# Performance work log

Measured on AMD Instinct MI355X. Metric: run time of the kernel, lower is better.

## Reference

```python
import jax, jax.numpy as jnp
import numpy as np

LENGTHS = [1024, 768, 896, 512, 1024, 640, 1024, 768, 512, 896, 1024, 704]  # sum = 9792
EMBED, HEADS = 1024, 16
HDIM = EMBED // HEADS  # 64
ROPE_BASE = 10000.0


def _rotate_half(x):
    half = x.shape[-1] // 2
    return jnp.concatenate([-x[..., half:], x[..., :half]], axis=-1)


def setup_inputs() -> dict:
    key = jax.random.key(0)
    ks = jax.random.split(key, 8)
    T = sum(LENGTHS)
    hidden = jax.random.normal(ks[0], (T, EMBED), jnp.float32)
    # RoPE cos/sin: positions restart at 0 within each packed segment
    pos = np.concatenate([np.arange(l) for l in LENGTHS]).astype(np.float32)  # [T]
    inv_freq = 1.0 / (ROPE_BASE ** (np.arange(0, HDIM, 2, dtype=np.float32) / HDIM))
    freqs = np.outer(pos, inv_freq)                       # [T, HDIM//2]
    emb = np.concatenate([freqs, freqs], axis=-1)         # [T, HDIM]
    cos = jnp.asarray(np.cos(emb), jnp.float32)
    sin = jnp.asarray(np.sin(emb), jnp.float32)
    s = 0.02
    q_w = jax.random.normal(ks[1], (EMBED, EMBED), jnp.float32) * s
    k_w = jax.random.normal(ks[2], (EMBED, EMBED), jnp.float32) * s
    v_w = jax.random.normal(ks[3], (EMBED, EMBED), jnp.float32) * s
    out_w = jax.random.normal(ks[4], (EMBED, EMBED), jnp.float32) * s
    q_b = jax.random.normal(ks[5], (EMBED,), jnp.float32) * s
    v_b = jax.random.normal(ks[6], (EMBED,), jnp.float32) * s
    out_b = jax.random.normal(ks[7], (EMBED,), jnp.float32) * s
    return {
        "hidden_states": hidden, "cos": cos, "sin": sin,
        "q_w": q_w, "q_b": q_b, "k_w": k_w, "v_w": v_w, "v_b": v_b,
        "out_w": out_w, "out_b": out_b,
        "seq_len": jnp.array(LENGTHS, jnp.int32),
        "max_seqlen": 1024,
    }


def reference(hidden_states, cos, sin, q_w, q_b, k_w, v_w, v_b, out_w, out_b,
              seq_len, max_seqlen):
    T, D = hidden_states.shape
    H, Dh = HEADS, D // HEADS
    B = seq_len.shape[0]
    L = max_seqlen  # static python int

    # Projections (torch Linear: y = x @ W.T + b; k_proj has no bias)
    q = (hidden_states @ q_w.T + q_b).reshape(T, H, Dh)
    k = (hidden_states @ k_w.T).reshape(T, H, Dh)
    v = (hidden_states @ v_w.T + v_b).reshape(T, H, Dh)

    # Inline RoPE (cos/sin broadcast over heads)
    c = cos[:, None, :]
    s = sin[:, None, :]
    q = q * c + _rotate_half(q) * s
    k = k * c + _rotate_half(k) * s

    # Gather packed tokens into padded [B, L, H, Dh] (honors ragged structure:
    # no [T, T] dense score matrix, only per-segment [L, L] blocks)
    cu = jnp.concatenate([jnp.zeros((1,), seq_len.dtype), jnp.cumsum(seq_len)])[:-1]  # [B] starts
    ar = jnp.arange(L)
    idx = cu[:, None] + ar[None, :]                 # [B, L] token ids
    valid = ar[None, :] < seq_len[:, None]          # [B, L]
    idxc = jnp.minimum(idx, T - 1)
    qp = q[idxc]                                    # [B, L, H, Dh]
    kp = k[idxc]
    vp = v[idxc]

    scale = 1.0 / jnp.sqrt(jnp.float32(Dh))
    scores = jnp.einsum('blhd,bmhd->bhlm', qp, kp) * scale  # [B, H, L, L]
    causal = ar[:, None] >= ar[None, :]             # [L, L]
    mask = valid[:, None, None, :] & causal[None, None, :, :]
    scores = jnp.where(mask, scores, jnp.float32(-1e30))
    probs = jax.nn.softmax(scores, axis=-1)
    attn = jnp.einsum('bhlm,bmhd->blhd', probs, vp).reshape(B, L, D)

    # Scatter valid tokens back to packed layout [T, D]
    attn = attn * valid[..., None].astype(attn.dtype)
    flat = jnp.zeros((T, D), attn.dtype).at[idxc.reshape(-1)].add(attn.reshape(-1, D))
    return flat @ out_w.T + out_b
```

## Files before the change

kernel.cpp:

```cpp
#include <hip/hip_runtime.h>

typedef __bf16 bf16;
typedef __bf16 bf16x8 __attribute__((ext_vector_type(8)));
typedef __bf16 bf16x4 __attribute__((ext_vector_type(4)));
typedef float  f32x4  __attribute__((ext_vector_type(4)));

#define T_TOTAL 9792
#define EMBED   1024
#define NHEAD   16
#define HDIM    64

__constant__ int c_seq_start[12] = {0,1024,1792,2688,3200,4224,4864,5888,6656,7168,8064,9088};
__constant__ int c_tiles_cum[13] = {0,16,28,42,50,66,76,92,104,112,126,142,153};

typedef __attribute__((address_space(1))) unsigned int gu32;
typedef __attribute__((address_space(3))) unsigned int lu32;

__device__ __forceinline__ void load_lds16(const void* g, void* l) {
    __builtin_amdgcn_global_load_lds((gu32*)g, (lu32*)l, 16, 0, 0);
}

__device__ __forceinline__ f32x4 mfma16(bf16x8 a, bf16x8 b, f32x4 c) {
    return __builtin_amdgcn_mfma_f32_16x16x32_bf16(a, b, c, 0, 0, 0);
}

struct CvtArgs {
    const void* src[10];
    bf16*       dst[10];
    int         n[10];
    int         cum[10];
};

__global__ void to_bf16_fused(CvtArgs a, const unsigned short* __restrict__ disc)
{
    const bool f32 = (disc[0] == 0);
    const int blk = blockIdx.x;
    int seg = 0;
    #pragma unroll
    for (int i = 1; i < 10; ++i) if (blk >= a.cum[i]) seg = i;
    int i0 = (blk - a.cum[seg]) * 2048 + threadIdx.x * 8;
    if (i0 >= a.n[seg]) return;
    bf16x8 o;
    if (f32) {
        const float4* s = (const float4*)((const float*)a.src[seg] + i0);
        float4 x = s[0], y = s[1];
        o[0]=(bf16)x.x; o[1]=(bf16)x.y; o[2]=(bf16)x.z; o[3]=(bf16)x.w;
        o[4]=(bf16)y.x; o[5]=(bf16)y.y; o[6]=(bf16)y.z; o[7]=(bf16)y.w;
    } else {
        o = *(const bf16x8*)((const bf16*)a.src[seg] + i0);
    }
    *(bf16x8*)(a.dst[seg] + i0) = o;
}

__device__ __forceinline__
void gemm_core(const bf16* __restrict__ A, const bf16* __restrict__ W,
               int M, int m0, int n0, f32x4 (&acc)[4][4],
               bf16* lA, bf16* lB)
{
    const int tid  = threadIdx.x;
    const int wave = tid >> 6, lane = tid & 63;
    const int lrow = lane >> 3;
    const int gsw  = (lane & 7) ^ lrow;
    const int ln   = lane & 15, lq = lane >> 4;
    const int e7   = ln & 7;
    const int wm = (wave & 1) * 64,  wn = (wave >> 1) * 64;

    for (int k0 = 0; k0 < 1024; k0 += 64) {
        __syncthreads();
        for (int j = 0; j < 4; ++j) {
            int r = j * 32 + wave * 8;
            int gr = m0 + r + lrow; if (gr > M - 1) gr = M - 1;
            load_lds16(A + (size_t)gr * EMBED + k0 + gsw * 8, &lA[r * 64]);
            load_lds16(W + (size_t)(n0 + r + lrow) * EMBED + k0 + gsw * 8, &lB[r * 64]);
        }
        __syncthreads();
        #pragma unroll
        for (int kb = 0; kb < 2; ++kb) {
            bf16x8 af[4], bfr[4];
            #pragma unroll
            for (int i = 0; i < 4; ++i)
                af[i]  = *(const bf16x8*)&lA[(wm + i * 16 + ln) * 64 + (((kb * 4 + lq) ^ e7) * 8)];
            #pragma unroll
            for (int i = 0; i < 4; ++i)
                bfr[i] = *(const bf16x8*)&lB[(wn + i * 16 + ln) * 64 + (((kb * 4 + lq) ^ e7) * 8)];
            #pragma unroll
            for (int mi = 0; mi < 4; ++mi)
                #pragma unroll
                for (int ni = 0; ni < 4; ++ni)
                    acc[mi][ni] = mfma16(af[mi], bfr[ni], acc[mi][ni]);
        }
    }
}

__device__ __forceinline__ void map_block(int L, int NY, int& x, int& y)
{
    const int per = 8 * NY;
    const int full = 9 * per;
    if (L < full) { int sc = L / per, rem = L % per; x = sc * 8 + (rem & 7); y = rem >> 3; }
    else          { int rem = L - full; x = 72 + rem % 5; y = rem / 5; }
}

__global__ __launch_bounds__(256, 2)
void gemm_qkv(const bf16* __restrict__ A,
              const bf16* __restrict__ Wq, const bf16* __restrict__ Wk,
              const bf16* __restrict__ Wv, const bf16* __restrict__ qb,
              const bf16* __restrict__ vb,
              const bf16* __restrict__ cosb, const bf16* __restrict__ sinb,
              bf16* __restrict__ Cq, bf16* __restrict__ Ck,
              bf16* __restrict__ Vt, int M)
{
    __shared__ __align__(16) bf16 lA[128 * 64];
    __shared__ __align__(16) bf16 lB[128 * 64];

    int x, yy;
    map_block(blockIdx.x, 24, x, yy);
    const int which = yy >> 3;
    const int m0 = x * 128, n0 = (yy & 7) * 128;

    const bf16* W = (which == 0) ? Wq : (which == 1) ? Wk : Wv;
    f32x4 acc[4][4] = {};
    gemm_core(A, W, M, m0, n0, acc, lA, lB);

    const int tid  = threadIdx.x;
    const int wave = tid >> 6, lane = tid & 63;
    const int ln   = lane & 15, lq = lane >> 4;
    const int wm = (wave & 1) * 64,  wn = (wave >> 1) * 64;

    if (which < 2) {
        bf16* C = (which == 0) ? Cq : Ck;
        const bf16* bias = (which == 0) ? qb : nullptr;
        #pragma unroll
        for (int mi = 0; mi < 4; ++mi) {
            int trow = m0 + wm + mi * 16 + lq * 4;
            if (trow >= M) continue;
            #pragma unroll
            for (int ni = 0; ni < 2; ++ni) {
                int d    = ni * 16 + ln;
                int col0 = n0 + wn + d;
                int col1 = col0 + 32;
                float b0 = bias ? (float)bias[col0] : 0.0f;
                float b1 = bias ? (float)bias[col1] : 0.0f;
                #pragma unroll
                for (int r = 0; r < 4; ++r) {
                    int t = trow + r;
                    float c = (float)cosb[t * HDIM + d];
                    float s = (float)sinb[t * HDIM + d];
                    float x0 = acc[mi][ni][r] + b0;
                    float x1 = acc[mi][ni + 2][r] + b1;
                    C[(size_t)t * EMBED + col0] = (bf16)(x0 * c - x1 * s);
                    C[(size_t)t * EMBED + col1] = (bf16)(x1 * c + x0 * s);
                }
            }
        }
    } else {
        const int hd0 = n0 + wn;
        #pragma unroll
        for (int mi = 0; mi < 4; ++mi) {
            int trow = m0 + wm + mi * 16 + lq * 4;
            if (trow >= M) continue;
            #pragma unroll
            for (int ni = 0; ni < 4; ++ni) {
                int d = ni * 16 + ln;
                float bv = (float)vb[hd0 + d];
                bf16x4 o;
                #pragma unroll
                for (int r = 0; r < 4; ++r) o[r] = (bf16)(acc[mi][ni][r] + bv);
                *(bf16x4*)&Vt[(size_t)(hd0 + d) * T_TOTAL + trow] = o;
            }
        }
    }
}

__global__ __launch_bounds__(256, 2)
void gemm_out(const bf16* __restrict__ A, const bf16* __restrict__ W,
              const bf16* __restrict__ bias, void* __restrict__ out, int M,
              const unsigned short* __restrict__ disc)
{
    __shared__ __align__(16) bf16 lA[128 * 64];
    __shared__ __align__(16) bf16 lB[128 * 64];

    int x, yy;
    map_block(blockIdx.x, 8, x, yy);
    const int m0 = x * 128, n0 = yy * 128;

    f32x4 acc[4][4] = {};
    gemm_core(A, W, M, m0, n0, acc, lA, lB);

    const bool f32 = (disc[0] == 0);
    const int tid  = threadIdx.x;
    const int wave = tid >> 6, lane = tid & 63;
    const int ln   = lane & 15, lq = lane >> 4;
    const int wm = (wave & 1) * 64,  wn = (wave >> 1) * 64;

    #pragma unroll
    for (int mi = 0; mi < 4; ++mi) {
        int trow = m0 + wm + mi * 16 + lq * 4;
        if (trow >= M) continue;
        #pragma unroll
        for (int ni = 0; ni < 4; ++ni) {
            int col = n0 + wn + ni * 16 + ln;
            float bv = (float)bias[col];
            #pragma unroll
            for (int r = 0; r < 4; ++r) {
                float v = acc[mi][ni][r] + bv;
                size_t idx = (size_t)(trow + r) * EMBED + col;
                if (f32) ((float*)out)[idx] = v;
                else     ((bf16*)out)[idx]  = (bf16)v;
            }
        }
    }
}

__global__ __launch_bounds__(256, 3)
void attn_kernel(const bf16* __restrict__ Q, const bf16* __restrict__ K,
                 const bf16* __restrict__ Vt, bf16* __restrict__ O)
{
    __shared__ __align__(16) bf16 sK[2][64 * 64];
    __shared__ __align__(16) bf16 sV[2][64 * 64];
    __shared__ __align__(16) bf16 sQP[4 * 16 * 72];

    const int tid  = threadIdx.x;
    const int wave = tid >> 6, lane = tid & 63;
    const int lrow = lane >> 3;
    const int gsw  = (lane & 7) ^ lrow;
    const int ln   = lane & 15, lq = lane >> 4;
    const int e7   = ln & 7;
    const int h = blockIdx.y;

    int b = 0;
    #pragma unroll
    for (int i = 1; i < 13; ++i) if ((int)blockIdx.x >= c_tiles_cum[i]) b = i;
    const int qt = blockIdx.x - c_tiles_cum[b];
    const int t0 = c_seq_start[b] + qt * 64;
    const int kvb0 = c_seq_start[b];

    for (int p = 0; p < 2; ++p) {
        int r = p * 32 + wave * 8;
        load_lds16(Q  + (size_t)(t0 + r + lrow) * EMBED + h * HDIM + gsw * 8, &sQP[r * 64]);
        load_lds16(K  + (size_t)(kvb0 + r + lrow) * EMBED + h * HDIM + gsw * 8, &sK[0][r * 64]);
        load_lds16(Vt + (size_t)(h * HDIM + r + lrow) * T_TOTAL + kvb0 + gsw * 8, &sV[0][r * 64]);
    }

    bf16x8 qf[2];
    f32x4 oacc[4] = {};
    float m_i = -1e30f, l_i = 0.0f;
    const float sc = 0.125f * 1.44269504088896f;
    const int q_loc = wave * 16 + ln;
    bf16* sP = &sQP[wave * 16 * 72];

    for (int j = 0; j <= qt; ++j) {
        __syncthreads();
        const int cur = j & 1;
        if (j == 0) {
            qf[0] = *(const bf16x8*)&sQP[q_loc * 64 + ((0 + lq) ^ e7) * 8];
            qf[1] = *(const bf16x8*)&sQP[q_loc * 64 + ((4 + lq) ^ e7) * 8];
            __syncthreads();
        }
        if (j < qt) {
            const int kvb = kvb0 + (j + 1) * 64;
            const int nxt = cur ^ 1;
            for (int p = 0; p < 2; ++p) {
                int r = p * 32 + wave * 8;
                load_lds16(K  + (size_t)(kvb + r + lrow) * EMBED + h * HDIM + gsw * 8, &sK[nxt][r * 64]);
                load_lds16(Vt + (size_t)(h * HDIM + r + lrow) * T_TOTAL + kvb + gsw * 8, &sV[nxt][r * 64]);
            }
        }

        f32x4 s[4] = {};
        #pragma unroll
        for (int kk = 0; kk < 2; ++kk)
            #pragma unroll
            for (int ni = 0; ni < 4; ++ni) {
                bf16x8 kf = *(const bf16x8*)&sK[cur][(ni * 16 + ln) * 64 + (((kk * 4 + lq) ^ e7) * 8)];
                s[ni] = mfma16(kf, qf[kk], s[ni]);
            }

        float pb[4][4];
        if (j == qt) {
            #pragma unroll
            for (int ni = 0; ni < 4; ++ni)
                #pragma unroll
                for (int r = 0; r < 4; ++r) {
                    int kv = ni * 16 + lq * 4 + r;
                    pb[ni][r] = (kv <= q_loc) ? s[ni][r] * sc : -1e30f;
                }
        } else {
            #pragma unroll
            for (int ni = 0; ni < 4; ++ni)
                #pragma unroll
                for (int r = 0; r < 4; ++r)
                    pb[ni][r] = s[ni][r] * sc;
        }

        float mx = pb[0][0];
        #pragma unroll
        for (int ni = 0; ni < 4; ++ni)
            #pragma unroll
            for (int r = 0; r < 4; ++r) mx = fmaxf(mx, pb[ni][r]);
        mx = fmaxf(mx, __shfl_xor(mx, 16));
        mx = fmaxf(mx, __shfl_xor(mx, 32));
        float mnew  = fmaxf(m_i, mx);
        float alpha = exp2f(m_i - mnew);
        m_i = mnew;

        float rs = 0.0f;
        #pragma unroll
        for (int ni = 0; ni < 4; ++ni)
            #pragma unroll
            for (int r = 0; r < 4; ++r) {
                float pe = exp2f(pb[ni][r] - mnew);
                pb[ni][r] = pe;
                rs += pe;
            }
        rs += __shfl_xor(rs, 16);
        rs += __shfl_xor(rs, 32);
        l_i = l_i * alpha + rs;
        #pragma unroll
        for (int d = 0; d < 4; ++d)
            #pragma unroll
            for (int r = 0; r < 4; ++r) oacc[d][r] *= alpha;

        #pragma unroll
        for (int ni = 0; ni < 4; ++ni) {
            bf16x4 w4;
            #pragma unroll
            for (int r = 0; r < 4; ++r) w4[r] = (bf16)pb[ni][r];
            *(bf16x4*)&sP[ln * 72 + ni * 16 + lq * 4] = w4;
        }
        asm volatile("s_waitcnt lgkmcnt(0)" ::: "memory");

        #pragma unroll
        for (int kk = 0; kk < 2; ++kk) {
            bf16x8 pf = *(const bf16x8*)&sP[ln * 72 + kk * 32 + lq * 8];
            #pragma unroll
            for (int d = 0; d < 4; ++d) {
                bf16x8 vf = *(const bf16x8*)&sV[cur][(d * 16 + ln) * 64 + (((kk * 4 + lq) ^ e7) * 8)];
                oacc[d] = mfma16(vf, pf, oacc[d]);
            }
        }
    }

    const float inv = 1.0f / l_i;
    const size_t row = (size_t)(t0 + q_loc) * EMBED + h * HDIM;
    #pragma unroll
    for (int d = 0; d < 4; ++d) {
        bf16x4 o4;
        #pragma unroll
        for (int r = 0; r < 4; ++r) o4[r] = (bf16)(oacc[d][r] * inv);
        *(bf16x4*)&O[row + d * 16 + lq * 4] = o4;
    }
}

extern "C" void kernel_launch(void* const* d_in, const int* in_sizes, int n_in,
                              void* d_out, int out_size, void* d_ws, size_t ws_size,
                              hipStream_t stream)
{
    const unsigned short* disc = (const unsigned short*)d_in[1];

    const size_t SZ  = (size_t)T_TOTAL * EMBED;
    const size_t CS  = (size_t)T_TOTAL * HDIM;
    const size_t WSZ = (size_t)EMBED * EMBED;

    bf16* p = (bf16*)d_ws;
    bf16* ch   = p; p += SZ;
    bf16* ccos = p; p += CS;
    bf16* csin = p; p += CS;
    bf16* cqw  = p; p += WSZ;
    bf16* ckw  = p; p += WSZ;
    bf16* cvw  = p; p += WSZ;
    bf16* cow  = p; p += WSZ;
    bf16* cqb  = p; p += EMBED;
    bf16* cvb  = p; p += EMBED;
    bf16* cob  = p; p += EMBED;
    bf16* wq   = p; p += SZ;
    bf16* wk   = p; p += SZ;
    bf16* wvt  = p; p += SZ;

    CvtArgs ca;
    const void* srcs[10] = {d_in[0], d_in[1], d_in[2], d_in[3], d_in[5],
                            d_in[6], d_in[8], d_in[4], d_in[7], d_in[9]};
    bf16* dsts[10] = {ch, ccos, csin, cqw, ckw, cvw, cow, cqb, cvb, cob};
    int   ns[10]   = {(int)SZ, (int)CS, (int)CS, (int)WSZ, (int)WSZ,
                      (int)WSZ, (int)WSZ, EMBED, EMBED, EMBED};
    int cum = 0;
    for (int i = 0; i < 10; ++i) {
        ca.src[i] = srcs[i]; ca.dst[i] = dsts[i]; ca.n[i] = ns[i];
        ca.cum[i] = cum;
        cum += (ns[i] + 2047) / 2048;
    }
    to_bf16_fused<<<cum, 256, 0, stream>>>(ca, disc);

    gemm_qkv<<<77 * 24, 256, 0, stream>>>(ch, cqw, ckw, cvw, cqb, cvb,
                                          ccos, csin, wq, wk, wvt, T_TOTAL);
    attn_kernel<<<dim3(153, 16), 256, 0, stream>>>(wq, wk, wvt, wq);
    gemm_out<<<77 * 8, 256, 0, stream>>>(wq, cow, cob, d_out, T_TOTAL, disc);
}
```

Measured before the change: 297.0 us.

## Use 256x256 double-buffered GEMM tiles with 8 waves for QKV and output projections

Both projection GEMMs move from 128x128 tiles on 4 waves to 256x256 tiles on 8 waves. LDS is double-buffered so the next K-slice is prefetched during the MFMA phases, and MFMA issue is raised with setprio. The aim is more operand reuse per byte loaded and less barrier/load latency exposed. In exchange the grids shrink sharply (156 blocks for the output GEMM), 128 KB of LDS limits each CU to one block, and tail waves may leave CUs idle.

```diff
diff --git a/kernel.cpp b/kernel.cpp
--- a/kernel.cpp
+++ b/kernel.cpp
@@ -52,10 +52,23 @@
     *(bf16x8*)(a.dst[seg] + i0) = o;
 }
 
+__device__ __forceinline__ void map_block2(int L, int NX, int NY, int& x, int& y)
+{
+    const int per = 8 * NY;
+    const int nfull = NX >> 3;
+    const int full = nfull * per;
+    if (L < full) { int sc = L / per, rem = L % per; x = sc * 8 + (rem & 7); y = rem >> 3; }
+    else {
+        int rem = L - full;
+        int tw = NX - nfull * 8;
+        x = nfull * 8 + rem % tw; y = rem / tw;
+    }
+}
+
 __device__ __forceinline__
-void gemm_core(const bf16* __restrict__ A, const bf16* __restrict__ W,
-               int M, int m0, int n0, f32x4 (&acc)[4][4],
-               bf16* lA, bf16* lB)
+void gemm_core256(const bf16* __restrict__ A, const bf16* __restrict__ W,
+                  int M, int m0, int n0, f32x4 (&acc)[8][4],
+                  bf16* lA, bf16* lB)
 {
     const int tid  = threadIdx.x;
     const int wave = tid >> 6, lane = tid & 63;
@@ -63,44 +76,66 @@
     const int gsw  = (lane & 7) ^ lrow;
     const int ln   = lane & 15, lq = lane >> 4;
     const int e7   = ln & 7;
-    const int wm = (wave & 1) * 64,  wn = (wave >> 1) * 64;
-
-    for (int k0 = 0; k0 < 1024; k0 += 64) {
-        __syncthreads();
+    const int wm   = (wave >> 2) & 1;
+    const int wn   = wave & 3;
+
+    auto stage = [&](int kt, int buf) {
+        const int k0 = kt * 64;
+        bf16* dA = lA + buf * (256 * 64);
+        bf16* dB = lB + buf * (256 * 64);
+        #pragma unroll
         for (int j = 0; j < 4; ++j) {
-            int r = j * 32 + wave * 8;
+            int r = j * 64 + wave * 8;
             int gr = m0 + r + lrow; if (gr > M - 1) gr = M - 1;
-            load_lds16(A + (size_t)gr * EMBED + k0 + gsw * 8, &lA[r * 64]);
-            load_lds16(W + (size_t)(n0 + r + lrow) * EMBED + k0 + gsw * 8, &lB[r * 64]);
-        }
-        __syncthreads();
-        #pragma unroll
-        for (int kb = 0; kb < 2; ++kb) {
-            bf16x8 af[4], bfr[4];
-            #pragma unroll
-            for (int i = 0; i < 4; ++i)
-                af[i]  = *(const bf16x8*)&lA[(wm + i * 16 + ln) * 64 + (((kb * 4 + lq) ^ e7) * 8)];
-            #pragma unroll
-            for (int i = 0; i < 4; ++i)
-                bfr[i] = *(const bf16x8*)&lB[(wn + i * 16 + ln) * 64 + (((kb * 4 + lq) ^ e7) * 8)];
-            #pragma unroll
-            for (int mi = 0; mi < 4; ++mi)
-                #pragma unroll
-                for (int ni = 0; ni < 4; ++ni)
-                    acc[mi][ni] = mfma16(af[mi], bfr[ni], acc[mi][ni]);
-        }
-    }
-}
-
-__device__ __forceinline__ void map_block(int L, int NY, int& x, int& y)
-{
-    const int per = 8 * NY;
-    const int full = 9 * per;
-    if (L < full) { int sc = L / per, rem = L % per; x = sc * 8 + (rem & 7); y = rem >> 3; }
-    else          { int rem = L - full; x = 72 + rem % 5; y = rem / 5; }
-}
-
-__global__ __launch_bounds__(256, 2)
+            load_lds16(A + (size_t)gr * EMBED + k0 + gsw * 8, dA + r * 64);
+            load_lds16(W + (size_t)(n0 + r + lrow) * EMBED + k0 + gsw * 8, dB + r * 64);
+        }
+    };
+
+    stage(0, 0);
+    __syncthreads();
+
+    for (int kt = 0; kt < 16; ++kt) {
+        const int p = kt & 1;
+        const bf16* sA = lA + p * (256 * 64);
+        const bf16* sB = lB + p * (256 * 64);
+        #pragma unroll
+        for (int ph = 0; ph < 4; ++ph) {
+            const int mh = ph >> 1, nh = ph & 1;
+            if (ph == 0 && kt + 1 < 16) stage(kt + 1, p ^ 1);
+
+            bf16x8 af[2][4], bfr[2][2];
+            #pragma unroll
+            for (int kb = 0; kb < 2; ++kb) {
+                #pragma unroll
+                for (int mi = 0; mi < 4; ++mi)
+                    af[kb][mi] = *(const bf16x8*)
+                        &sA[(wm * 128 + mh * 64 + mi * 16 + ln) * 64 + (((kb * 4 + lq) ^ e7) * 8)];
+                #pragma unroll
+                for (int niq = 0; niq < 2; ++niq)
+                    bfr[kb][niq] = *(const bf16x8*)
+                        &sB[(wn * 64 + nh * 32 + niq * 16 + ln) * 64 + (((kb * 4 + lq) ^ e7) * 8)];
+            }
+            __builtin_amdgcn_s_barrier();
+            asm volatile("s_waitcnt lgkmcnt(0)" ::: "memory");
+            __builtin_amdgcn_s_setprio(1);
+            #pragma unroll
+            for (int kb = 0; kb < 2; ++kb)
+                #pragma unroll
+                for (int mi = 0; mi < 4; ++mi)
+                    #pragma unroll
+                    for (int niq = 0; niq < 2; ++niq)
+                        acc[mh * 4 + mi][nh * 2 + niq] =
+                            mfma16(af[kb][mi], bfr[kb][niq], acc[mh * 4 + mi][nh * 2 + niq]);
+            __builtin_amdgcn_s_setprio(0);
+            if (ph == 3 && kt + 1 < 16)
+                asm volatile("s_waitcnt vmcnt(0)" ::: "memory");
+            __builtin_amdgcn_s_barrier();
+        }
+    }
+}
+
+__global__ __launch_bounds__(512, 2)
 void gemm_qkv(const bf16* __restrict__ A,
               const bf16* __restrict__ Wq, const bf16* __restrict__ Wk,
               const bf16* __restrict__ Wv, const bf16* __restrict__ qb,
@@ -109,34 +144,36 @@
               bf16* __restrict__ Cq, bf16* __restrict__ Ck,
               bf16* __restrict__ Vt, int M)
 {
-    __shared__ __align__(16) bf16 lA[128 * 64];
-    __shared__ __align__(16) bf16 lB[128 * 64];
+    __shared__ __align__(16) bf16 lA[2 * 256 * 64];
+    __shared__ __align__(16) bf16 lB[2 * 256 * 64];
 
     int x, yy;
-    map_block(blockIdx.x, 24, x, yy);
-    const int which = yy >> 3;
-    const int m0 = x * 128, n0 = (yy & 7) * 128;
+    map_block2(blockIdx.x, 39, 12, x, yy);
+    const int which = yy >> 2;
+    const int m0 = x * 256, n0 = (yy & 3) * 256;
 
     const bf16* W = (which == 0) ? Wq : (which == 1) ? Wk : Wv;
-    f32x4 acc[4][4] = {};
-    gemm_core(A, W, M, m0, n0, acc, lA, lB);
+    f32x4 acc[8][4] = {};
+    gemm_core256(A, W, M, m0, n0, acc, lA, lB);
 
     const int tid  = threadIdx.x;
     const int wave = tid >> 6, lane = tid & 63;
     const int ln   = lane & 15, lq = lane >> 4;
-    const int wm = (wave & 1) * 64,  wn = (wave >> 1) * 64;
+    const int wm   = (wave >> 2) & 1, wn = wave & 3;
+    const int rbase = m0 + wm * 128;
+    const int cbase = n0 + wn * 64;
 
     if (which < 2) {
         bf16* C = (which == 0) ? Cq : Ck;
         const bf16* bias = (which == 0) ? qb : nullptr;
         #pragma unroll
-        for (int mi = 0; mi < 4; ++mi) {
-            int trow = m0 + wm + mi * 16 + lq * 4;
+        for (int mi = 0; mi < 8; ++mi) {
+            int trow = rbase + mi * 16 + lq * 4;
             if (trow >= M) continue;
             #pragma unroll
             for (int ni = 0; ni < 2; ++ni) {
                 int d    = ni * 16 + ln;
-                int col0 = n0 + wn + d;
+                int col0 = cbase + d;
                 int col1 = col0 + 32;
                 float b0 = bias ? (float)bias[col0] : 0.0f;
                 float b1 = bias ? (float)bias[col1] : 0.0f;
@@ -153,52 +190,53 @@
             }
         }
     } else {
-        const int hd0 = n0 + wn;
-        #pragma unroll
-        for (int mi = 0; mi < 4; ++mi) {
-            int trow = m0 + wm + mi * 16 + lq * 4;
+        #pragma unroll
+        for (int mi = 0; mi < 8; ++mi) {
+            int trow = rbase + mi * 16 + lq * 4;
             if (trow >= M) continue;
             #pragma unroll
             for (int ni = 0; ni < 4; ++ni) {
                 int d = ni * 16 + ln;
-                float bv = (float)vb[hd0 + d];
+                float bv = (float)vb[cbase + d];
                 bf16x4 o;
                 #pragma unroll
                 for (int r = 0; r < 4; ++r) o[r] = (bf16)(acc[mi][ni][r] + bv);
-                *(bf16x4*)&Vt[(size_t)(hd0 + d) * T_TOTAL + trow] = o;
-            }
-        }
-    }
-}
-
-__global__ __launch_bounds__(256, 2)
+                *(bf16x4*)&Vt[(size_t)(cbase + d) * T_TOTAL + trow] = o;
+            }
+        }
+    }
+}
+
+__global__ __launch_bounds__(512, 2)
 void gemm_out(const bf16* __restrict__ A, const bf16* __restrict__ W,
               const bf16* __restrict__ bias, void* __restrict__ out, int M,
               const unsigned short* __restrict__ disc)
 {
-    __shared__ __align__(16) bf16 lA[128 * 64];
-    __shared__ __align__(16) bf16 lB[128 * 64];
+    __shared__ __align__(16) bf16 lA[2 * 256 * 64];
+    __shared__ __align__(16) bf16 lB[2 * 256 * 64];
 
     int x, yy;
-    map_block(blockIdx.x, 8, x, yy);
-    const int m0 = x * 128, n0 = yy * 128;
-
-    f32x4 acc[4][4] = {};
-    gemm_core(A, W, M, m0, n0, acc, lA, lB);
+    map_block2(blockIdx.x, 39, 4, x, yy);
+    const int m0 = x * 256, n0 = yy * 256;
+
+    f32x4 acc[8][4] = {};
+    gemm_core256(A, W, M, m0, n0, acc, lA, lB);
 
     const bool f32 = (disc[0] == 0);
     const int tid  = threadIdx.x;
     const int wave = tid >> 6, lane = tid & 63;
     const int ln   = lane & 15, lq = lane >> 4;
-    const int wm = (wave & 1) * 64,  wn = (wave >> 1) * 64;
+    const int wm   = (wave >> 2) & 1, wn = wave & 3;
+    const int rbase = m0 + wm * 128;
+    const int cbase = n0 + wn * 64;
 
     #pragma unroll
-    for (int mi = 0; mi < 4; ++mi) {
-        int trow = m0 + wm + mi * 16 + lq * 4;
+    for (int mi = 0; mi < 8; ++mi) {
+        int trow = rbase + mi * 16 + lq * 4;
         if (trow >= M) continue;
         #pragma unroll
         for (int ni = 0; ni < 4; ++ni) {
-            int col = n0 + wn + ni * 16 + ln;
+            int col = cbase + ni * 16 + ln;
             float bv = (float)bias[col];
             #pragma unroll
             for (int r = 0; r < 4; ++r) {
@@ -390,8 +428,8 @@
     }
     to_bf16_fused<<<cum, 256, 0, stream>>>(ca, disc);
 
-    gemm_qkv<<<77 * 24, 256, 0, stream>>>(ch, cqw, ckw, cvw, cqb, cvb,
+    gemm_qkv<<<39 * 12, 512, 0, stream>>>(ch, cqw, ckw, cvw, cqb, cvb,
                                           ccos, csin, wq, wk, wvt, T_TOTAL);
     attn_kernel<<<dim3(153, 16), 256, 0, stream>>>(wq, wk, wvt, wq);
-    gemm_out<<<77 * 8, 256, 0, stream>>>(wq, cow, cob, d_out, T_TOTAL, disc);
-}
+    gemm_out<<<39 * 4, 512, 0, stream>>>(wq, cow, cob, d_out, T_TOTAL, disc);
+}
```

After: 331.4 us. 1.12x slower.

## Pipeline GEMM mainloop with 4-stage LDS ring and async prefetch

Applied to the files above, without the earlier changes.

Replaces the synchronous two-barrier GEMM mainloop used by the QKV and output projections with a 4-buffer LDS ring of 32-wide K slices. Three stages are prefetched via global_load_lds, and explicit vmcnt waits plus a single barrier per iteration let loads overlap MFMA work. MFMA issue is wrapped in s_setprio. LDS per block grows to 64 KB, which could limit occupancy at the declared 2 blocks per CU, and the hand-counted waitcnt values must match the outstanding loads exactly.

```diff
diff --git a/kernel.cpp b/kernel.cpp
--- a/kernel.cpp
+++ b/kernel.cpp
@@ -52,52 +52,72 @@
     *(bf16x8*)(a.dst[seg] + i0) = o;
 }
 
-__device__ __forceinline__
-void gemm_core(const bf16* __restrict__ A, const bf16* __restrict__ W,
-               int M, int m0, int n0, f32x4 (&acc)[4][4],
-               bf16* lA, bf16* lB)
-{
-    const int tid  = threadIdx.x;
-    const int wave = tid >> 6, lane = tid & 63;
-    const int lrow = lane >> 3;
-    const int gsw  = (lane & 7) ^ lrow;
-    const int ln   = lane & 15, lq = lane >> 4;
-    const int e7   = ln & 7;
-    const int wm = (wave & 1) * 64,  wn = (wave >> 1) * 64;
-
-    for (int k0 = 0; k0 < 1024; k0 += 64) {
-        __syncthreads();
-        for (int j = 0; j < 4; ++j) {
-            int r = j * 32 + wave * 8;
-            int gr = m0 + r + lrow; if (gr > M - 1) gr = M - 1;
-            load_lds16(A + (size_t)gr * EMBED + k0 + gsw * 8, &lA[r * 64]);
-            load_lds16(W + (size_t)(n0 + r + lrow) * EMBED + k0 + gsw * 8, &lB[r * 64]);
-        }
-        __syncthreads();
-        #pragma unroll
-        for (int kb = 0; kb < 2; ++kb) {
-            bf16x8 af[4], bfr[4];
-            #pragma unroll
-            for (int i = 0; i < 4; ++i)
-                af[i]  = *(const bf16x8*)&lA[(wm + i * 16 + ln) * 64 + (((kb * 4 + lq) ^ e7) * 8)];
-            #pragma unroll
-            for (int i = 0; i < 4; ++i)
-                bfr[i] = *(const bf16x8*)&lB[(wn + i * 16 + ln) * 64 + (((kb * 4 + lq) ^ e7) * 8)];
-            #pragma unroll
-            for (int mi = 0; mi < 4; ++mi)
-                #pragma unroll
-                for (int ni = 0; ni < 4; ++ni)
-                    acc[mi][ni] = mfma16(af[mi], bfr[ni], acc[mi][ni]);
-        }
-    }
-}
-
 __device__ __forceinline__ void map_block(int L, int NY, int& x, int& y)
 {
     const int per = 8 * NY;
     const int full = 9 * per;
     if (L < full) { int sc = L / per, rem = L % per; x = sc * 8 + (rem & 7); y = rem >> 3; }
     else          { int rem = L - full; x = 72 + rem % 5; y = rem / 5; }
+}
+
+__device__ __forceinline__
+void gemm_core128(const bf16* __restrict__ A, const bf16* __restrict__ W,
+                  int M, int m0, int n0, f32x4 (&acc)[4][4], bf16* lds)
+{
+    const int tid  = threadIdx.x;
+    const int wave = tid >> 6, lane = tid & 63;
+    const int ln   = lane & 15, lq = lane >> 4;
+    const int wm   = (wave & 1) * 64, wn = (wave >> 1) * 64;
+
+    const int sgsw = ((tid & 3) ^ ((tid >> 3) & 3)) * 8;
+    int rr0 = m0 + (tid >> 2);       if (rr0 > M - 1) rr0 = M - 1;
+    int rr1 = m0 + 64 + (tid >> 2);  if (rr1 > M - 1) rr1 = M - 1;
+    const bf16* gA0 = A + (size_t)rr0 * EMBED + sgsw;
+    const bf16* gA1 = A + (size_t)rr1 * EMBED + sgsw;
+    const bf16* gB0 = W + (size_t)(n0 + (tid >> 2)) * EMBED + sgsw;
+    const bf16* gB1 = W + (size_t)(n0 + 64 + (tid >> 2)) * EMBED + sgsw;
+
+    auto stage = [&](int t) {
+        const int k0 = t * 32;
+        bf16* dA = lds + (t & 3) * 8192;
+        bf16* dB = dA + 4096;
+        load_lds16(gA0 + k0, dA + tid * 8);
+        load_lds16(gA1 + k0, dA + 2048 + tid * 8);
+        load_lds16(gB0 + k0, dB + tid * 8);
+        load_lds16(gB1 + k0, dB + 2048 + tid * 8);
+    };
+
+    stage(0); stage(1); stage(2);
+
+    const int rsw  = (lq ^ ((ln >> 1) & 3)) * 8;
+    const int aoff = (wm + ln) * 32 + rsw;
+    const int boff = (wn + ln) * 32 + rsw;
+
+    for (int t = 0; t < 32; ++t) {
+        if (t < 30)       asm volatile("s_waitcnt vmcnt(8)" ::: "memory");
+        else if (t == 30) asm volatile("s_waitcnt vmcnt(4)" ::: "memory");
+        else              asm volatile("s_waitcnt vmcnt(0)" ::: "memory");
+        asm volatile("s_barrier" ::: "memory");
+        if (t + 3 < 32) stage(t + 3);
+
+        const bf16* sA = lds + (t & 3) * 8192;
+        const bf16* sB = sA + 4096;
+        bf16x8 af[4], bfr[4];
+        #pragma unroll
+        for (int mi = 0; mi < 4; ++mi)
+            af[mi]  = *(const bf16x8*)&sA[aoff + mi * 512];
+        #pragma unroll
+        for (int ni = 0; ni < 4; ++ni)
+            bfr[ni] = *(const bf16x8*)&sB[boff + ni * 512];
+
+        __builtin_amdgcn_s_setprio(1);
+        #pragma unroll
+        for (int mi = 0; mi < 4; ++mi)
+            #pragma unroll
+            for (int ni = 0; ni < 4; ++ni)
+                acc[mi][ni] = mfma16(af[mi], bfr[ni], acc[mi][ni]);
+        __builtin_amdgcn_s_setprio(0);
+    }
 }
 
 __global__ __launch_bounds__(256, 2)
@@ -109,8 +129,7 @@
               bf16* __restrict__ Cq, bf16* __restrict__ Ck,
               bf16* __restrict__ Vt, int M)
 {
-    __shared__ __align__(16) bf16 lA[128 * 64];
-    __shared__ __align__(16) bf16 lB[128 * 64];
+    __shared__ __align__(16) bf16 lds[4 * 8192];
 
     int x, yy;
     map_block(blockIdx.x, 24, x, yy);
@@ -119,7 +138,7 @@
 
     const bf16* W = (which == 0) ? Wq : (which == 1) ? Wk : Wv;
     f32x4 acc[4][4] = {};
-    gemm_core(A, W, M, m0, n0, acc, lA, lB);
+    gemm_core128(A, W, M, m0, n0, acc, lds);
 
     const int tid  = threadIdx.x;
     const int wave = tid >> 6, lane = tid & 63;
@@ -176,15 +195,14 @@
               const bf16* __restrict__ bias, void* __restrict__ out, int M,
               const unsigned short* __restrict__ disc)
 {
-    __shared__ __align__(16) bf16 lA[128 * 64];
-    __shared__ __align__(16) bf16 lB[128 * 64];
+    __shared__ __align__(16) bf16 lds[4 * 8192];
 
     int x, yy;
     map_block(blockIdx.x, 8, x, yy);
     const int m0 = x * 128, n0 = yy * 128;
 
     f32x4 acc[4][4] = {};
-    gemm_core(A, W, M, m0, n0, acc, lA, lB);
+    gemm_core128(A, W, M, m0, n0, acc, lds);
 
     const bool f32 = (disc[0] == 0);
     const int tid  = threadIdx.x;
```

Result: slower. 309.7 us (+4.3%).
